# Kernel tuning notes

Hardware: AMD Instinct MI355X
Metric: run time of the kernel (lower is better)

## Reference

```python
import jax, jax.numpy as jnp
import numpy as np

N_NODES, N_EDGES, N_GRAPHS = 100000, 1600000, 1000
HID, GRP = 64, 10
LAMDA, EPS, T = 0.01, 1e-5, 2  # DiffGroupNorm lambda, BN eps, num_timesteps


def seg_softmax(logits, seg, num_segments):
    m = jax.ops.segment_max(logits, seg, num_segments=num_segments)
    e = jnp.exp(logits - m[seg])
    s = jax.ops.segment_sum(e, seg, num_segments=num_segments)
    return e / (s[seg] + 1e-16)


def gatv2(x_src, x_dst, src, dst, e_emb, Wl, bl, Wr, br, att, bias, n_dst):
    # GATv2Conv, heads=1, add_self_loops=False, negative_slope=0.01, aggr='add'
    xl = x_src @ Wl + bl                      # source transform (lin_l)
    xr = x_dst @ Wr + br                      # target transform (lin_r)
    m = xl[src] + xr[dst]                     # [E, C]
    if e_emb is not None:
        m = m + e_emb
    m = jnp.where(m > 0, m, 0.01 * m)         # leaky_relu(0.01)
    a = seg_softmax(m @ att, dst, n_dst)      # softmax over in-edges of each target
    out = jax.ops.segment_sum(xl[src] * a[:, None], dst, n_dst)
    return out + bias


def gru(xi, h, Wih, Whh, bih, bhh):
    gi = xi @ Wih.T + bih
    gh = h @ Whh.T + bhh
    ir, iz, inn = jnp.split(gi, 3, axis=-1)
    hr, hz, hn = jnp.split(gh, 3, axis=-1)
    r = jax.nn.sigmoid(ir + hr)
    z = jax.nn.sigmoid(iz + hz)
    n = jnp.tanh(inn + r * hn)
    return (1.0 - z) * n + z * h


def diff_group_norm(x, lin_W, lin_b, bn_w, bn_b):
    # PyG DiffGroupNorm (training-mode BatchNorm1d over groups*F)
    n, f = x.shape
    s = jax.nn.softmax(x @ lin_W + lin_b, axis=-1)            # [N, G]
    out = (s[:, :, None] * x[:, None, :]).reshape(n, GRP * f)  # [N, G*F]
    mean = out.mean(0)
    var = ((out - mean) ** 2).mean(0)
    out = (out - mean) / jnp.sqrt(var + EPS) * bn_w + bn_b
    out = out.reshape(n, GRP, f).sum(1)
    return x + LAMDA * out


def forward(x, edge_index, edge_attr, batch, pre_nW, pre_nb, pre_eW, pre_eb,
            g_Wl, g_Wl_b, g_Wr, g_Wr_b, g_We, g_att, g_bias,
            gru_Wih, gru_Whh, gru_bih, gru_bhh, gn_W, gn_b, bn_w, bn_b,
            ggat_Wl, ggat_Wl_b, ggat_Wr, ggat_Wr_b, ggat_att, ggat_bias,
            ggru_Wih, ggru_Whh, ggru_bih, ggru_bhh, ggn_W, ggn_b, gbn_w, gbn_b,
            post_W, post_b, out_W, out_b):
    src, dst = edge_index[0], edge_index[1]
    x = jax.nn.relu(x @ pre_nW + pre_nb)
    e = jax.nn.relu(edge_attr @ pre_eW + pre_eb)
    for l in range(g_Wl.shape[0]):            # layers_attention - 1 = 2 blocks
        e_emb = e @ g_We[l]                   # lin_edge (no bias)
        for _ in range(T):
            h = jax.nn.elu(gatv2(x, x, src, dst, e_emb, g_Wl[l], g_Wl_b[l],
                                 g_Wr[l], g_Wr_b[l], g_att[l], g_bias[l], N_NODES))
            x = jax.nn.relu(gru(h, x, gru_Wih[l], gru_Whh[l], gru_bih[l], gru_bhh[l]))
        x = diff_group_norm(x, gn_W[l], gn_b[l], bn_w[l], bn_b[l])
    # global readout: bipartite graph nodes -> graphs
    rsrc = jnp.arange(N_NODES)
    out = jax.nn.relu(jax.ops.segment_sum(x, batch, num_segments=N_GRAPHS))
    for _ in range(T):
        h = jax.nn.elu(gatv2(x, out, rsrc, batch, None, ggat_Wl, ggat_Wl_b,
                             ggat_Wr, ggat_Wr_b, ggat_att, ggat_bias, N_GRAPHS))
        out = jax.nn.relu(gru(h, out, ggru_Wih, ggru_Whh, ggru_bih, ggru_bhh))
    y = diff_group_norm(out, ggn_W, ggn_b, gbn_w, gbn_b)
    for l in range(post_W.shape[0]):
        y = jax.nn.relu(y @ post_W[l] + post_b[l])
    y = y @ out_W + out_b
    return y.reshape(-1)


def setup_inputs() -> dict:
    key = jax.random.key(0)
    ks = iter(jax.random.split(key, 64))
    Fin, Fe, H, L = 92, 50, HID, 2
    def nrm(shape, s=0.1):
        return jax.random.normal(next(ks), shape, jnp.float32) * s
    d = dict(
        x=jax.random.normal(next(ks), (N_NODES, Fin), jnp.float32),
        edge_index=jax.random.randint(next(ks), (2, N_EDGES), 0, N_NODES),
        edge_attr=jax.random.normal(next(ks), (N_EDGES, Fe), jnp.float32),
        batch=jnp.sort(jax.random.randint(next(ks), (N_NODES,), 0, N_GRAPHS)),
        pre_nW=nrm((Fin, H)), pre_nb=nrm((H,)),
        pre_eW=nrm((Fe, H)), pre_eb=nrm((H,)),
        g_Wl=nrm((L, H, H)), g_Wl_b=nrm((L, H)),
        g_Wr=nrm((L, H, H)), g_Wr_b=nrm((L, H)),
        g_We=nrm((L, H, H)), g_att=nrm((L, H)), g_bias=nrm((L, H)),
        gru_Wih=nrm((L, 3 * H, H)), gru_Whh=nrm((L, 3 * H, H)),
        gru_bih=nrm((L, 3 * H)), gru_bhh=nrm((L, 3 * H)),
        gn_W=nrm((L, H, GRP)), gn_b=nrm((L, GRP)),
        bn_w=jnp.ones((L, GRP * H), jnp.float32), bn_b=jnp.zeros((L, GRP * H), jnp.float32),
        ggat_Wl=nrm((H, H)), ggat_Wl_b=nrm((H,)),
        ggat_Wr=nrm((H, H)), ggat_Wr_b=nrm((H,)),
        ggat_att=nrm((H,)), ggat_bias=nrm((H,)),
        ggru_Wih=nrm((3 * H, H)), ggru_Whh=nrm((3 * H, H)),
        ggru_bih=nrm((3 * H,)), ggru_bhh=nrm((3 * H,)),
        ggn_W=nrm((H, GRP)), ggn_b=nrm((GRP,)),
        gbn_w=jnp.ones((GRP * H,), jnp.float32), gbn_b=jnp.zeros((GRP * H,), jnp.float32),
        post_W=nrm((2, H, H)), post_b=nrm((2, H)),
        out_W=nrm((H, 1)), out_b=nrm((1,)),
    )
    return d


def reference(x, edge_index, edge_attr, batch, pre_nW, pre_nb, pre_eW, pre_eb,
              g_Wl, g_Wl_b, g_Wr, g_Wr_b, g_We, g_att, g_bias,
              gru_Wih, gru_Whh, gru_bih, gru_bhh, gn_W, gn_b, bn_w, bn_b,
              ggat_Wl, ggat_Wl_b, ggat_Wr, ggat_Wr_b, ggat_att, ggat_bias,
              ggru_Wih, ggru_Whh, ggru_bih, ggru_bhh, ggn_W, ggn_b, gbn_w, gbn_b,
              post_W, post_b, out_W, out_b):
    return forward(x, edge_index, edge_attr, batch, pre_nW, pre_nb, pre_eW, pre_eb,
                   g_Wl, g_Wl_b, g_Wr, g_Wr_b, g_We, g_att, g_bias,
                   gru_Wih, gru_Whh, gru_bih, gru_bhh, gn_W, gn_b, bn_w, bn_b,
                   ggat_Wl, ggat_Wl_b, ggat_Wr, ggat_Wr_b, ggat_att, ggat_bias,
                   ggru_Wih, ggru_Whh, ggru_bih, ggru_bhh, ggn_W, ggn_b, gbn_w, gbn_b,
                   post_W, post_b, out_W, out_b)
```

## Files before the change

### kernel.cpp

```cpp
#include <hip/hip_runtime.h>
#include <hip/hip_bf16.h>

#define N_NODES 100000
#define N_EDGES 1600000
#define N_GRAPHS 1000
#define HID 64
#define GRP 10

typedef __attribute__((ext_vector_type(8))) short bf16x8;
typedef __attribute__((ext_vector_type(4))) float f32x4;

__device__ __forceinline__ float bf1(unsigned short u){ union{unsigned int x; float f;} v; v.x = ((unsigned int)u)<<16; return v.f; }
__device__ __forceinline__ float bf_lo(unsigned int u){ union{unsigned int x; float f;} v; v.x = u<<16; return v.f; }
__device__ __forceinline__ float bf_hi(unsigned int u){ union{unsigned int x; float f;} v; v.x = u & 0xFFFF0000u; return v.f; }
__device__ __forceinline__ unsigned short f2bf(float f){
  union{float f; unsigned int i;} v; v.f = f;
  unsigned int r = v.i + 0x7FFFu + ((v.i >> 16) & 1u);
  return (unsigned short)(r >> 16);
}
__device__ __forceinline__ float eluf(float v){ return v > 0.f ? v : expm1f(v); }
__device__ __forceinline__ float sigf(float v){ return 1.f/(1.f + expf(-v)); }

struct CvtEnt { const float* s; float* d; int rows; int cols; };
struct CvtArgs { CvtEnt e[16]; int cnt; };

__global__ __launch_bounds__(256) void k_convert(CvtArgs a){
  CvtEnt E = a.e[blockIdx.y];
  int n = E.rows * E.cols;
  for (int i = blockIdx.x*256 + threadIdx.x; i < n; i += gridDim.x*256){
    int r = i / E.cols, c = i % E.cols;
    E.d[(size_t)c*E.rows + r] = E.s[i];
  }
}

struct SpEnt { const float* s; unsigned short* dhi; unsigned short* dlo; int n; int k; int trans; };
struct SpArgs { SpEnt e[12]; int cnt; };

__global__ __launch_bounds__(256) void k_wsplit(SpArgs a){
  SpEnt E = a.e[blockIdx.y];
  int tot = E.n * E.k;
  for (int i = blockIdx.x*256 + threadIdx.x; i < tot; i += gridDim.x*256){
    int nr = i / E.k, kc = i - nr*E.k;
    float v = E.trans ? E.s[(size_t)kc*E.n + nr] : E.s[i];
    unsigned short hi = f2bf(v);
    unsigned short lo = f2bf(v - bf1(hi));
    E.dhi[i] = hi; E.dlo[i] = lo;
  }
}

__global__ __launch_bounds__(256) void k_wprep(const float* __restrict__ W1,
  const float* __restrict__ W2a, const float* __restrict__ W2b,
  unsigned short* __restrict__ W1Tb, unsigned short* __restrict__ W2Tba,
  unsigned short* __restrict__ W2Tbb)
{
  int i = blockIdx.x*256 + threadIdx.x;
  if (i >= 4096) return;
  int out = i & 63, k = i >> 6;
  int ks = k < 50 ? k : 0;
  unsigned short v1 = f2bf(W1[ks*64 + out]);
  if (k >= 50) v1 = 0;
  W1Tb [out*64 + k] = v1;
  W2Tba[out*64 + k] = f2bf(W2a[k*64 + out]);
  W2Tbb[out*64 + k] = f2bf(W2b[k*64 + out]);
}

__global__ __launch_bounds__(256) void k_hist(const int* __restrict__ dst, int* __restrict__ cnt){
  for (int e = blockIdx.x*256 + threadIdx.x; e < N_EDGES; e += gridDim.x*256)
    atomicAdd(cnt + dst[e], 1);
}

__global__ __launch_bounds__(256) void k_scan1(const int* __restrict__ cnt,
  int* __restrict__ excl, int* __restrict__ bsum, int N)
{
  __shared__ int sh[256];
  int t = threadIdx.x;
  int i = blockIdx.x*256 + t;
  int v = (i < N) ? cnt[i] : 0;
  sh[t] = v;
  __syncthreads();
  #pragma unroll
  for (int o=1;o<256;o<<=1){
    int x = (t>=o) ? sh[t-o] : 0;
    __syncthreads();
    sh[t] += x;
    __syncthreads();
  }
  if (i < N) excl[i] = sh[t] - v;
  if (t == 255) bsum[blockIdx.x] = sh[255];
}

__global__ __launch_bounds__(512) void k_scan2(const int* __restrict__ bsum,
  int* __restrict__ bo, int NB)
{
  __shared__ int sh[512];
  int t = threadIdx.x;
  int v = (t < NB) ? bsum[t] : 0;
  sh[t] = v;
  __syncthreads();
  #pragma unroll
  for (int o=1;o<512;o<<=1){
    int x = (t>=o) ? sh[t-o] : 0;
    __syncthreads();
    sh[t] += x;
    __syncthreads();
  }
  if (t < NB) bo[t] = sh[t] - v;
}

__global__ __launch_bounds__(256) void k_scan3(int* __restrict__ segoff,
  const int* __restrict__ bo, int* __restrict__ cursor, int N)
{
  int i = blockIdx.x*256 + threadIdx.x;
  if (i >= N) return;
  int v = segoff[i] + bo[i>>8];
  segoff[i] = v;
  cursor[i] = v;
  if (i == 0) segoff[N] = N_EDGES;
}

__global__ __launch_bounds__(256) void k_scatter(const int* __restrict__ src,
  const int* __restrict__ dst, int* __restrict__ cursor,
  int* __restrict__ srcp, int* __restrict__ perm)
{
  for (int e = blockIdx.x*256 + threadIdx.x; e < N_EDGES; e += gridDim.x*256){
    int d = dst[e];
    int pos = atomicAdd(cursor + d, 1);
    srcp[pos] = src[e];
    perm[pos] = e;
  }
}

__global__ __launch_bounds__(256) void k_goff(const int* __restrict__ batch, int* __restrict__ goff){
  for (int n = blockIdx.x*256 + threadIdx.x; n < N_NODES; n += gridDim.x*256){
    int b = batch[n];
    int prev = (n==0) ? -1 : batch[n-1];
    for (int g = prev+1; g <= b; g++) goff[g] = n;
    if (n == N_NODES-1){ for (int g=b+1; g<=N_GRAPHS; g++) goff[g] = N_NODES; }
  }
}

__global__ __launch_bounds__(256) void k_edge_emb(
  const float* __restrict__ EA, const int* __restrict__ perm,
  const unsigned short* __restrict__ W1Tb,
  const float* __restrict__ b1, const unsigned short* __restrict__ W2Tb,
  unsigned short* __restrict__ out, int nTiles)
{
  __shared__ float ea[64*50];
  __shared__ unsigned short hb[64*72];

  int tid = threadIdx.x;
  int lane = tid & 63;
  int wave = tid >> 6;
  int row16 = lane & 15;
  int kg = lane >> 4;

  bf16x8 w1[4][2], w2[4][2];
  #pragma unroll
  for (int n=0;n<4;n++){
    #pragma unroll
    for (int kk=0;kk<2;kk++){
      w1[n][kk] = *(const bf16x8*)(W1Tb + (n*16+row16)*64 + kk*32 + kg*8);
      w2[n][kk] = *(const bf16x8*)(W2Tb + (n*16+row16)*64 + kk*32 + kg*8);
    }
  }
  float bias[4];
  #pragma unroll
  for (int n=0;n<4;n++) bias[n] = b1[n*16+row16];

  int r = wave*16 + row16;
  float2 st[7];

  {
    long tile = blockIdx.x;
    if (tile < nTiles){
      #pragma unroll
      for (int k=0;k<7;k++){
        int j = tid + (k<<8);
        if (j < 1600){
          int row = j/25, c2 = j - row*25;
          int p = perm[tile*64 + row];
          st[k] = *(const float2*)(EA + (size_t)p*50 + (c2<<1));
        }
      }
    }
  }

  for (long t = blockIdx.x; t < nTiles; t += gridDim.x){
    #pragma unroll
    for (int k=0;k<7;k++){
      int j = tid + (k<<8);
      if (j < 1600){
        int row = j/25, c2 = j - row*25;
        *(float2*)(ea + row*50 + (c2<<1)) = st[k];
      }
    }
    __syncthreads();
    long tn = t + gridDim.x;
    if (tn < nTiles){
      #pragma unroll
      for (int k=0;k<7;k++){
        int j = tid + (k<<8);
        if (j < 1600){
          int row = j/25, c2 = j - row*25;
          int p = perm[tn*64 + row];
          st[k] = *(const float2*)(EA + (size_t)p*50 + (c2<<1));
        }
      }
    }

    bf16x8 a0, a1;
    {
      const float* p = ea + r*50;
      #pragma unroll
      for (int i=0;i<8;i++) ((short*)&a0)[i] = (short)f2bf(p[kg*8+i]);
      #pragma unroll
      for (int i=0;i<8;i++){
        int k = 32 + kg*8 + i;
        ((short*)&a1)[i] = (short)((k < 50) ? f2bf(p[k]) : (unsigned short)0);
      }
    }
    f32x4 c[4];
    #pragma unroll
    for (int n=0;n<4;n++){
      f32x4 acc = {0.f,0.f,0.f,0.f};
      acc = __builtin_amdgcn_mfma_f32_16x16x32_bf16(a0, w1[n][0], acc, 0,0,0);
      acc = __builtin_amdgcn_mfma_f32_16x16x32_bf16(a1, w1[n][1], acc, 0,0,0);
      c[n] = acc;
    }
    #pragma unroll
    for (int n=0;n<4;n++){
      #pragma unroll
      for (int q=0;q<4;q++){
        float v = fmaxf(c[n][q] + bias[n], 0.f);
        hb[(wave*16 + kg*4 + q)*72 + n*16 + row16] = f2bf(v);
      }
    }
    __syncthreads();

    bf16x8 ha = *(const bf16x8*)(hb + r*72 + kg*8);
    bf16x8 hc = *(const bf16x8*)(hb + r*72 + 32 + kg*8);
    f32x4 d[4];
    #pragma unroll
    for (int n=0;n<4;n++){
      f32x4 acc = {0.f,0.f,0.f,0.f};
      acc = __builtin_amdgcn_mfma_f32_16x16x32_bf16(ha, w2[n][0], acc, 0,0,0);
      acc = __builtin_amdgcn_mfma_f32_16x16x32_bf16(hc, w2[n][1], acc, 0,0,0);
      d[n] = acc;
    }
    __syncthreads();
    #pragma unroll
    for (int n=0;n<4;n++){
      #pragma unroll
      for (int q=0;q<4;q++)
        hb[(wave*16 + kg*4 + q)*72 + n*16 + row16] = f2bf(d[n][q]);
    }
    __syncthreads();

    {
      int rr = tid >> 2, q = tid & 3;
      const uint4* sp = (const uint4*)(hb + rr*72 + (q<<4));
      uint4 v0 = sp[0], v1 = sp[1];
      uint4* gp = (uint4*)(out + (t*64 + rr)*64 + (q<<4));
      gp[0] = v0; gp[1] = v1;
    }
  }
}

__device__ __forceinline__ void pack4(unsigned short* hi, unsigned short* lo, int ofs,
                                      float v0, float v1, float v2, float v3){
  unsigned short h0=f2bf(v0), h1=f2bf(v1), h2=f2bf(v2), h3=f2bf(v3);
  unsigned short l0=f2bf(v0-bf1(h0)), l1=f2bf(v1-bf1(h1)), l2=f2bf(v2-bf1(h2)), l3=f2bf(v3-bf1(h3));
  uint2 ph, pl;
  ph.x = ((unsigned int)h1<<16)|h0; ph.y = ((unsigned int)h3<<16)|h2;
  pl.x = ((unsigned int)l1<<16)|l0; pl.y = ((unsigned int)l3<<16)|l2;
  *(uint2*)(hi + ofs) = ph;
  *(uint2*)(lo + ofs) = pl;
}

template<int DUAL, int RELU>
__global__ __launch_bounds__(256) void k_lin_mfma(
  const float* __restrict__ X,
  const unsigned short* __restrict__ WAhi, const unsigned short* __restrict__ WAlo,
  const float* __restrict__ bA, float* __restrict__ outA,
  const unsigned short* __restrict__ WBhi, const unsigned short* __restrict__ WBlo,
  const float* __restrict__ bB, float* __restrict__ outB, int N)
{
  __shared__ unsigned short xh[64*72], xlo[64*72];
  int tid = threadIdx.x, lane = tid & 63, wave = tid >> 6;
  int col = lane & 15, kg = lane >> 4;
  long base = (long)blockIdx.x * 64;

  for (int idx = tid; idx < 1024; idx += 256){
    int r = idx >> 4, q = idx & 15;
    long row = base + r;
    float4 v = {0,0,0,0};
    if (row < N) v = ((const float4*)X)[row*16 + q];
    pack4(xh, xlo, r*72 + q*4, v.x, v.y, v.z, v.w);
  }
  __syncthreads();

  int r = wave*16 + col;
  bf16x8 ah[2], al[2];
  ah[0] = *(const bf16x8*)(xh  + r*72 + kg*8);
  ah[1] = *(const bf16x8*)(xh  + r*72 + 32 + kg*8);
  al[0] = *(const bf16x8*)(xlo + r*72 + kg*8);
  al[1] = *(const bf16x8*)(xlo + r*72 + 32 + kg*8);

  #pragma unroll
  for (int ct = 0; ct < 4; ct++){
    f32x4 aA = {0,0,0,0}, aB = {0,0,0,0};
    #pragma unroll
    for (int kk = 0; kk < 2; kk++){
      int wofs = (ct*16 + col)*64 + kk*32 + kg*8;
      bf16x8 bh = *(const bf16x8*)(WAhi + wofs);
      bf16x8 bl = *(const bf16x8*)(WAlo + wofs);
      aA = __builtin_amdgcn_mfma_f32_16x16x32_bf16(ah[kk], bh, aA, 0,0,0);
      aA = __builtin_amdgcn_mfma_f32_16x16x32_bf16(al[kk], bh, aA, 0,0,0);
      aA = __builtin_amdgcn_mfma_f32_16x16x32_bf16(ah[kk], bl, aA, 0,0,0);
      if (DUAL){
        bf16x8 ch = *(const bf16x8*)(WBhi + wofs);
        bf16x8 cl = *(const bf16x8*)(WBlo + wofs);
        aB = __builtin_amdgcn_mfma_f32_16x16x32_bf16(ah[kk], ch, aB, 0,0,0);
        aB = __builtin_amdgcn_mfma_f32_16x16x32_bf16(al[kk], ch, aB, 0,0,0);
        aB = __builtin_amdgcn_mfma_f32_16x16x32_bf16(ah[kk], cl, aB, 0,0,0);
      }
    }
    int c = ct*16 + col;
    float bAv = bA[c];
    float bBv = DUAL ? bB[c] : 0.f;
    #pragma unroll
    for (int reg = 0; reg < 4; reg++){
      long gr = base + wave*16 + kg*4 + reg;
      if (gr < N){
        float vA = aA[reg] + bAv;
        if (RELU) vA = fmaxf(vA, 0.f);
        outA[gr*64 + c] = vA;
        if (DUAL){
          float vB = aB[reg] + bBv;
          if (RELU) vB = fmaxf(vB, 0.f);
          outB[gr*64 + c] = vB;
        }
      }
    }
  }
}

__global__ __launch_bounds__(256) void k_gru_mfma(
  const float* __restrict__ agg, const float* __restrict__ gatb,
  float* __restrict__ x,
  const unsigned short* __restrict__ Wih_hi, const unsigned short* __restrict__ Wih_lo,
  const unsigned short* __restrict__ Whh_hi, const unsigned short* __restrict__ Whh_lo,
  const float* __restrict__ bih, const float* __restrict__ bhh, int N)
{
  __shared__ unsigned short hh_[64*72], hl_[64*72], xh_[64*72], xl_[64*72];
  int tid = threadIdx.x, lane = tid & 63, wave = tid >> 6;
  int col = lane & 15, kg = lane >> 4;
  long base = (long)blockIdx.x * 64;

  for (int idx = tid; idx < 1024; idx += 256){
    int r = idx >> 4, q = idx & 15;
    long row = base + r;
    float4 a = {0,0,0,0}, xx = {0,0,0,0};
    if (row < N){
      a  = ((const float4*)agg)[row*16 + q];
      xx = ((const float4*)x)[row*16 + q];
    }
    float h0 = eluf(a.x + gatb[q*4+0]);
    float h1 = eluf(a.y + gatb[q*4+1]);
    float h2 = eluf(a.z + gatb[q*4+2]);
    float h3 = eluf(a.w + gatb[q*4+3]);
    pack4(hh_, hl_, r*72 + q*4, h0, h1, h2, h3);
    pack4(xh_, xl_, r*72 + q*4, xx.x, xx.y, xx.z, xx.w);
  }
  __syncthreads();

  int r = wave*16 + col;
  bf16x8 hhi[2], hlo[2], xhi[2], xlo2[2];
  hhi[0] = *(const bf16x8*)(hh_ + r*72 + kg*8);
  hhi[1] = *(const bf16x8*)(hh_ + r*72 + 32 + kg*8);
  hlo[0] = *(const bf16x8*)(hl_ + r*72 + kg*8);
  hlo[1] = *(const bf16x8*)(hl_ + r*72 + 32 + kg*8);
  xhi[0] = *(const bf16x8*)(xh_ + r*72 + kg*8);
  xhi[1] = *(const bf16x8*)(xh_ + r*72 + 32 + kg*8);
  xlo2[0] = *(const bf16x8*)(xl_ + r*72 + kg*8);
  xlo2[1] = *(const bf16x8*)(xl_ + r*72 + 32 + kg*8);

  #pragma unroll
  for (int ct = 0; ct < 4; ct++){
    f32x4 ai[3], ah[3];
    #pragma unroll
    for (int g=0; g<3; g++){ ai[g] = (f32x4){0,0,0,0}; ah[g] = (f32x4){0,0,0,0}; }
    #pragma unroll
    for (int g = 0; g < 3; g++){
      int nt = g*4 + ct;
      #pragma unroll
      for (int kk = 0; kk < 2; kk++){
        int wofs = (nt*16 + col)*64 + kk*32 + kg*8;
        bf16x8 bh = *(const bf16x8*)(Wih_hi + wofs);
        bf16x8 bl = *(const bf16x8*)(Wih_lo + wofs);
        ai[g] = __builtin_amdgcn_mfma_f32_16x16x32_bf16(hhi[kk], bh, ai[g], 0,0,0);
        ai[g] = __builtin_amdgcn_mfma_f32_16x16x32_bf16(hlo[kk], bh, ai[g], 0,0,0);
        ai[g] = __builtin_amdgcn_mfma_f32_16x16x32_bf16(hhi[kk], bl, ai[g], 0,0,0);
        bf16x8 ch = *(const bf16x8*)(Whh_hi + wofs);
        bf16x8 cl = *(const bf16x8*)(Whh_lo + wofs);
        ah[g] = __builtin_amdgcn_mfma_f32_16x16x32_bf16(xhi[kk], ch, ah[g], 0,0,0);
        ah[g] = __builtin_amdgcn_mfma_f32_16x16x32_bf16(xlo2[kk], ch, ah[g], 0,0,0);
        ah[g] = __builtin_amdgcn_mfma_f32_16x16x32_bf16(xhi[kk], cl, ah[g], 0,0,0);
      }
    }
    int c = ct*16 + col;
    float bi0 = bih[c], bi1 = bih[64+c], bi2 = bih[128+c];
    float bh0 = bhh[c], bh1 = bhh[64+c], bh2 = bhh[128+c];
    #pragma unroll
    for (int reg = 0; reg < 4; reg++){
      int rr = wave*16 + kg*4 + reg;
      long gr = base + rr;
      float ir = ai[0][reg] + bi0, iz = ai[1][reg] + bi1, in2 = ai[2][reg] + bi2;
      float hr = ah[0][reg] + bh0, hz = ah[1][reg] + bh1, hn = ah[2][reg] + bh2;
      float xv = bf1(xh_[rr*72 + c]) + bf1(xl_[rr*72 + c]);
      float r_ = sigf(ir + hr);
      float z  = sigf(iz + hz);
      float nn = tanhf(in2 + r_*hn);
      float o = (1.f - z)*nn + z*xv;
      if (gr < N) x[gr*64 + c] = fmaxf(o, 0.f);
    }
  }
}

template<int K, int RELU, int INBF, int OUTBF, int HASB>
__global__ __launch_bounds__(256) void k_linear64(const void* Ap,
    const float* __restrict__ WT, const float* __restrict__ bias, void* Op, int N)
{
  int n = blockIdx.x*256 + threadIdx.x;
  if (n >= N) return;
  float a[K];
  if constexpr (INBF){
    const unsigned int* p = (const unsigned int*)((const unsigned short*)Ap + (size_t)n*K);
    #pragma unroll
    for (int i=0;i<K/2;i++){ unsigned int u=p[i]; a[2*i]=bf_lo(u); a[2*i+1]=bf_hi(u); }
  } else if constexpr (K % 4 == 0){
    const float4* p = (const float4*)((const float*)Ap + (size_t)n*K);
    #pragma unroll
    for (int i=0;i<K/4;i++){ float4 v=p[i]; a[4*i]=v.x; a[4*i+1]=v.y; a[4*i+2]=v.z; a[4*i+3]=v.w; }
  } else {
    const float2* p = (const float2*)((const float*)Ap + (size_t)n*K);
    #pragma unroll
    for (int i=0;i<K/2;i++){ float2 v=p[i]; a[2*i]=v.x; a[2*i+1]=v.y; }
  }
  for (int c=0;c<64;c+=4){
    float s0 = HASB ? bias[c+0] : 0.f;
    float s1 = HASB ? bias[c+1] : 0.f;
    float s2 = HASB ? bias[c+2] : 0.f;
    float s3 = HASB ? bias[c+3] : 0.f;
    const float* w = WT + (size_t)c*K;
    #pragma unroll
    for (int k=0;k<K;k++){
      float av = a[k];
      s0 = fmaf(av, w[k],     s0);
      s1 = fmaf(av, w[K+k],   s1);
      s2 = fmaf(av, w[2*K+k], s2);
      s3 = fmaf(av, w[3*K+k], s3);
    }
    if (RELU){ s0=fmaxf(s0,0.f); s1=fmaxf(s1,0.f); s2=fmaxf(s2,0.f); s3=fmaxf(s3,0.f); }
    if constexpr (OUTBF){
      uint2 uu;
      uu.x = ((unsigned int)f2bf(s1)<<16) | f2bf(s0);
      uu.y = ((unsigned int)f2bf(s3)<<16) | f2bf(s2);
      *(uint2*)((unsigned short*)Op + (size_t)n*64 + c) = uu;
    } else {
      float4 r; r.x=s0; r.y=s1; r.z=s2; r.w=s3;
      *(float4*)((float*)Op + (size_t)n*64 + c) = r;
    }
  }
}

template<int HASEMB, int IDSRC>
__global__ __launch_bounds__(256) void k_gat_fused(
  const int* __restrict__ srcp, const int* __restrict__ segoff,
  const float* __restrict__ xl, const float* __restrict__ xr,
  const unsigned short* __restrict__ emb, const float* __restrict__ att,
  float* __restrict__ agg, int nseg)
{
  int lane = threadIdx.x & 63;
  float av = att[lane];
  int wid = (blockIdx.x*256 + threadIdx.x) >> 6;
  int nw  = (gridDim.x*256) >> 6;
  for (int d = wid; d < nseg; d += nw){
    int e0 = segoff[d], e1 = segoff[d+1];
    float xrv = xr[(size_t)d*64 + lane];
    float m = -3.0e38f, s = 0.f, acc = 0.f;
    int e = e0;
    for (; e + 2 <= e1; e += 2){
      int sA = IDSRC ? e   : srcp[e];
      int sB = IDSRC ? e+1 : srcp[e+1];
      float xsA = xl[(size_t)sA*64 + lane];
      float xsB = xl[(size_t)sB*64 + lane];
      float vA = xsA + xrv, vB = xsB + xrv;
      if (HASEMB){
        vA += bf1(emb[(size_t)e*64 + lane]);
        vB += bf1(emb[(size_t)(e+1)*64 + lane]);
      }
      vA = vA > 0.f ? vA : 0.01f*vA;
      vB = vB > 0.f ? vB : 0.01f*vB;
      float pA = vA * av, pB = vB * av;
      #pragma unroll
      for (int o=32;o;o>>=1){ pA += __shfl_xor(pA, o, 64); pB += __shfl_xor(pB, o, 64); }
      float mn = fmaxf(m, fmaxf(pA, pB));
      float cm = expf(m - mn);
      float cA = expf(pA - mn);
      float cB = expf(pB - mn);
      s = fmaf(s, cm, cA + cB);
      acc = fmaf(acc, cm, fmaf(cA, xsA, cB*xsB));
      m = mn;
    }
    if (e < e1){
      int sN = IDSRC ? e : srcp[e];
      float xs = xl[(size_t)sN*64 + lane];
      float v = xs + xrv;
      if (HASEMB) v += bf1(emb[(size_t)e*64 + lane]);
      v = v > 0.f ? v : 0.01f*v;
      float p = v * av;
      #pragma unroll
      for (int o=32;o;o>>=1) p += __shfl_xor(p, o, 64);
      float mn = fmaxf(m, p);
      float cm = expf(m - mn);
      float cp = expf(p - mn);
      s   = fmaf(s, cm, cp);
      acc = fmaf(acc, cm, cp*xs);
      m = mn;
    }
    agg[(size_t)d*64 + lane] = acc / (s + 1e-16f);
  }
}

__global__ __launch_bounds__(256) void k_dgn_s(const float* __restrict__ x,
  const float* __restrict__ WT , const float* __restrict__ b,
  float* __restrict__ s, int N)
{
  int n = blockIdx.x*256 + threadIdx.x;
  if (n >= N) return;
  float a[64];
  const float4* p = (const float4*)(x + (size_t)n*64);
  #pragma unroll
  for (int i=0;i<16;i++){ float4 v=p[i]; a[4*i]=v.x; a[4*i+1]=v.y; a[4*i+2]=v.z; a[4*i+3]=v.w; }
  float lg[10];
  #pragma unroll
  for (int g=0; g<10; g++){
    float acc = b[g];
    const float* w = WT + (size_t)g*64;
    #pragma unroll
    for (int k=0;k<64;k++) acc = fmaf(a[k], w[k], acc);
    lg[g] = acc;
  }
  float m = lg[0];
  #pragma unroll
  for (int g=1;g<10;g++) m = fmaxf(m, lg[g]);
  float e[10], sum = 0.f;
  #pragma unroll
  for (int g=0;g<10;g++){ e[g] = expf(lg[g]-m); sum += e[g]; }
  float inv = 1.f/sum;
  #pragma unroll
  for (int g=0;g<10;g++) s[(size_t)n*10+g] = e[g]*inv;
}

__global__ __launch_bounds__(640) void k_dgn_stats(const float* __restrict__ s,
  const float* __restrict__ x, float* cs, float* cs2, int N)
{
  int g = threadIdx.x >> 6, f = threadIdx.x & 63;
  int per = (N + gridDim.x - 1) / gridDim.x;
  int n0 = blockIdx.x * per;
  int n1 = min(N, n0 + per);
  float a = 0.f, a2 = 0.f;
  for (int n = n0; n < n1; n++){
    float y = s[(size_t)n*10+g] * x[(size_t)n*64+f];
    a += y; a2 += y*y;
  }
  atomicAdd(&cs [g*64+f], a);
  atomicAdd(&cs2[g*64+f], a2);
}

__global__ void k_dgn_final(const float* cs, const float* cs2,
  const float* __restrict__ bw, const float* __restrict__ bb,
  float* scale, float* shiftsum, int N)
{
  __shared__ float sh[640];
  int i = threadIdx.x;
  float invN = 1.f / (float)N;
  float mean = cs[i]*invN;
  float var  = cs2[i]*invN - mean*mean;
  float sc = bw[i] / sqrtf(var + 1e-5f);
  scale[i] = sc;
  sh[i] = bb[i] - mean*sc;
  __syncthreads();
  if (i < 64){
    float t = 0.f;
    #pragma unroll
    for (int g=0;g<10;g++) t += sh[g*64+i];
    shiftsum[i] = t;
  }
}

__global__ __launch_bounds__(256) void k_dgn_apply(float* x,
  const float* __restrict__ s, const float* __restrict__ scale,
  const float* __restrict__ shiftsum, int N)
{
  int idx = blockIdx.x*256 + threadIdx.x;
  if (idx >= N*64) return;
  int n = idx >> 6, f = idx & 63;
  float ss = 0.f;
  #pragma unroll
  for (int g=0; g<10; g++) ss = fmaf(s[(size_t)n*10+g], scale[g*64+f], ss);
  float xvv = x[idx];
  x[idx] = xvv + 0.01f*(xvv*ss + shiftsum[f]);
}

__global__ __launch_bounds__(256) void k_gseg(const float* __restrict__ x,
  const int* __restrict__ goff, float* __restrict__ gout)
{
  int lane = threadIdx.x & 63;
  int wid = (blockIdx.x*256 + threadIdx.x) >> 6;
  int nw  = (gridDim.x*256) >> 6;
  for (int g = wid; g < N_GRAPHS; g += nw){
    int n0 = goff[g], n1 = goff[g+1];
    float acc = 0.f;
    for (int n = n0; n < n1; n++) acc += x[(size_t)n*64 + lane];
    gout[(size_t)g*64 + lane] = fmaxf(acc, 0.f);
  }
}

__global__ __launch_bounds__(256) void k_head(const float* __restrict__ y,
  const float* __restrict__ w, const float* __restrict__ b,
  float* __restrict__ out, int N)
{
  int n = blockIdx.x*256 + threadIdx.x;
  if (n >= N) return;
  float acc = b[0];
  const float4* p = (const float4*)(y + (size_t)n*64);
  #pragma unroll
  for (int i=0;i<16;i++){
    float4 v = p[i];
    acc = fmaf(v.x, w[4*i+0], acc);
    acc = fmaf(v.y, w[4*i+1], acc);
    acc = fmaf(v.z, w[4*i+2], acc);
    acc = fmaf(v.w, w[4*i+3], acc);
  }
  out[n] = acc;
}

extern "C" void kernel_launch(void* const* d_in, const int* in_sizes, int n_in,
                              void* d_out, int out_size, void* d_ws, size_t ws_size,
                              hipStream_t stream) {
  (void)in_sizes; (void)n_in; (void)out_size; (void)ws_size;

  char* base = (char*)d_ws; size_t off = 0;
  auto A = [&](size_t bytes)->void*{ void* p = base + off; off += (bytes + 255) & ~(size_t)255; return p; };
  unsigned short* e_emb = (unsigned short*)A((size_t)N_EDGES*64*2);
  float* xbuf   = (float*)A((size_t)N_NODES*64*4);
  float* xl     = (float*)A((size_t)N_NODES*64*4);
  float* xr     = (float*)A((size_t)N_NODES*64*4);
  float* agg    = (float*)A((size_t)N_NODES*64*4);
  int*   perm   = (int*)A((size_t)N_EDGES*4);
  int*   srcp   = (int*)A((size_t)N_EDGES*4);
  int*   segoff = (int*)A((size_t)(N_NODES+1)*4);
  int*   cursor = (int*)A((size_t)N_NODES*4);
  int*   bsum   = (int*)A(512*4);
  int*   bo     = (int*)A(512*4);
  int*   goff   = (int*)A((size_t)(N_GRAPHS+1)*4);
  float* sbuf   = (float*)A((size_t)N_NODES*10*4);
  float* gout   = (float*)A((size_t)N_GRAPHS*64*4);
  float* ybuf   = (float*)A((size_t)N_GRAPHS*64*4);
  float* ybuf2  = (float*)A((size_t)N_GRAPHS*64*4);
  float* colsum = (float*)A(2*640*4); float* colsumsq = colsum + 640;
  float* scale  = (float*)A((640+64)*4); float* shiftsum = scale + 640;
  unsigned short* W1Tb  = (unsigned short*)A(4096*2);
  unsigned short* W2Tb0 = (unsigned short*)A(4096*2);
  unsigned short* W2Tb1 = (unsigned short*)A(4096*2);
  unsigned short* LHI[5]; unsigned short* LLO[5];
  for (int i=0;i<5;i++){ LHI[i]=(unsigned short*)A(4096*2); LLO[i]=(unsigned short*)A(4096*2); }
  unsigned short* GHI[6]; unsigned short* GLO[6];
  for (int i=0;i<6;i++){ GHI[i]=(unsigned short*)A(12288*2); GLO[i]=(unsigned short*)A(12288*2); }
  float* wf     = (float*)A(60000*4);
  size_t wo = 0;
  auto W = [&](size_t n)->float*{ float* p = wf + wo; wo += n; return p; };

  float* pre_nWT = W(64*92);
  float* gnWT[2] = {W(640), W(640)};
  float* gWrT = W(4096);
  float* ggnWT = W(640);
  float* postWT[2] = {W(4096), W(4096)};

  const float* F[48];
  for (int i=0;i<41;i++) F[i] = (const float*)d_in[i];

  CvtArgs ca; ca.cnt = 0;
  auto addT = [&](const float* s, float* d, int r, int c){
    ca.e[ca.cnt].s=s; ca.e[ca.cnt].d=d; ca.e[ca.cnt].rows=r; ca.e[ca.cnt].cols=c; ca.cnt++; };

  addT(F[4],  pre_nWT, 92, 64);
  for (int l=0;l<2;l++) addT(F[19] + l*640,  gnWT[l], 64, 10);
  addT(F[25], gWrT, 64, 64);
  addT(F[33], ggnWT, 64, 10);
  for (int l=0;l<2;l++) addT(F[37] + l*4096, postWT[l], 64, 64);

  SpArgs sa; sa.cnt = 0;
  auto addS = [&](const float* s, unsigned short* dhi, unsigned short* dlo, int n, int k, int tr){
    sa.e[sa.cnt].s=s; sa.e[sa.cnt].dhi=dhi; sa.e[sa.cnt].dlo=dlo;
    sa.e[sa.cnt].n=n; sa.e[sa.cnt].k=k; sa.e[sa.cnt].trans=tr; sa.cnt++; };
  for (int l=0;l<2;l++) addS(F[8]  + l*4096, LHI[l],   LLO[l],   64, 64, 1);
  for (int l=0;l<2;l++) addS(F[10] + l*4096, LHI[2+l], LLO[2+l], 64, 64, 1);
  addS(F[23], LHI[4], LLO[4], 64, 64, 1);
  for (int l=0;l<2;l++) addS(F[15] + l*12288, GHI[l],   GLO[l],   192, 64, 0);
  for (int l=0;l<2;l++) addS(F[16] + l*12288, GHI[2+l], GLO[2+l], 192, 64, 0);
  addS(F[29], GHI[4], GLO[4], 192, 64, 0);
  addS(F[30], GHI[5], GLO[5], 192, 64, 0);

  const int* src   = (const int*)d_in[1];
  const int* dst   = src + N_EDGES;
  const int* batch = (const int*)d_in[3];

  const int NBn = (N_NODES + 255)/256;
  const int NBg = (N_GRAPHS + 255)/256;
  const int NBa = (N_NODES*64)/256;
  const int NTIL = N_EDGES/64;
  const int NBt = (N_NODES + 63)/64;
  const int NBtg = (N_GRAPHS + 63)/64;

  k_convert<<<dim3(24, ca.cnt), 256, 0, stream>>>(ca);
  k_wsplit<<<dim3(8, sa.cnt), 256, 0, stream>>>(sa);
  k_wprep<<<16,256,0,stream>>>(F[6], F[12], F[12]+4096, W1Tb, W2Tb0, W2Tb1);

  hipMemsetAsync(cursor, 0, (size_t)N_NODES*4, stream);
  k_hist<<<2048,256,0,stream>>>(dst, cursor);
  k_scan1<<<NBn,256,0,stream>>>(cursor, segoff, bsum, N_NODES);
  k_scan2<<<1,512,0,stream>>>(bsum, bo, NBn);
  k_scan3<<<NBn,256,0,stream>>>(segoff, bo, cursor, N_NODES);
  k_scatter<<<2048,256,0,stream>>>(src, dst, cursor, srcp, perm);
  k_goff<<<NBn,256,0,stream>>>(batch, goff);

  k_linear64<92,1,0,0,1><<<NBn,256,0,stream>>>(F[0], pre_nWT, F[5], xbuf, N_NODES);

  for (int l=0; l<2; l++){
    k_edge_emb<<<4096,256,0,stream>>>(F[2], perm, W1Tb, F[7], (l==0)?W2Tb0:W2Tb1, e_emb, NTIL);

    for (int t=0; t<2; t++){
      k_lin_mfma<1,0><<<NBt,256,0,stream>>>(xbuf,
          LHI[l], LLO[l], F[9] + l*64, xl,
          LHI[2+l], LLO[2+l], F[11] + l*64, xr, N_NODES);
      k_gat_fused<1,0><<<4096,256,0,stream>>>(srcp, segoff, xl, xr, e_emb,
                                              F[13] + l*64, agg, N_NODES);
      k_gru_mfma<<<NBt,256,0,stream>>>(agg, F[14] + l*64, xbuf,
          GHI[l], GLO[l], GHI[2+l], GLO[2+l],
          F[17] + l*192, F[18] + l*192, N_NODES);
    }
    hipMemsetAsync(colsum, 0, 2*640*4, stream);
    k_dgn_s<<<NBn,256,0,stream>>>(xbuf, gnWT[l], F[20] + l*10, sbuf, N_NODES);
    k_dgn_stats<<<512,640,0,stream>>>(sbuf, xbuf, colsum, colsumsq, N_NODES);
    k_dgn_final<<<1,640,0,stream>>>(colsum, colsumsq, F[21] + l*640, F[22] + l*640, scale, shiftsum, N_NODES);
    k_dgn_apply<<<NBa,256,0,stream>>>(xbuf, sbuf, scale, shiftsum, N_NODES);
  }

  k_gseg<<<250,256,0,stream>>>(xbuf, goff, gout);

  k_lin_mfma<0,0><<<NBt,256,0,stream>>>(xbuf, LHI[4], LLO[4], F[24], xl,
                                        nullptr, nullptr, nullptr, nullptr, N_NODES);
  for (int t=0; t<2; t++){
    k_linear64<64,0,0,0,1><<<NBg,256,0,stream>>>(gout, gWrT, F[26], xr, N_GRAPHS);
    k_gat_fused<0,1><<<256,256,0,stream>>>(nullptr, goff, xl, xr, nullptr,
                                           F[27], agg, N_GRAPHS);
    k_gru_mfma<<<NBtg,256,0,stream>>>(agg, F[28], gout,
        GHI[4], GLO[4], GHI[5], GLO[5], F[31], F[32], N_GRAPHS);
  }

  hipMemsetAsync(colsum, 0, 2*640*4, stream);
  k_dgn_s<<<NBg,256,0,stream>>>(gout, ggnWT, F[34], sbuf, N_GRAPHS);
  k_dgn_stats<<<8,640,0,stream>>>(sbuf, gout, colsum, colsumsq, N_GRAPHS);
  k_dgn_final<<<1,640,0,stream>>>(colsum, colsumsq, F[35], F[36], scale, shiftsum, N_GRAPHS);
  k_dgn_apply<<<(N_GRAPHS*64+255)/256,256,0,stream>>>(gout, sbuf, scale, shiftsum, N_GRAPHS);

  k_linear64<64,1,0,0,1><<<NBg,256,0,stream>>>(gout, postWT[0], F[38],      ybuf,  N_GRAPHS);
  k_linear64<64,1,0,0,1><<<NBg,256,0,stream>>>(ybuf, postWT[1], F[38] + 64, ybuf2, N_GRAPHS);
  k_head<<<NBg,256,0,stream>>>(ybuf2, F[39], F[40], (float*)d_out, N_GRAPHS);
}
```

Measured before the change: 2.930 ms.

## Read edge attrs contiguously with scattered emb writes; split GAT lanes across four edges

```diff
diff --git a/kernel.cpp b/kernel.cpp
--- a/kernel.cpp
+++ b/kernel.cpp
@@ -120,13 +120,13 @@
 
 __global__ __launch_bounds__(256) void k_scatter(const int* __restrict__ src,
   const int* __restrict__ dst, int* __restrict__ cursor,
-  int* __restrict__ srcp, int* __restrict__ perm)
+  int* __restrict__ srcp, int* __restrict__ ipos)
 {
   for (int e = blockIdx.x*256 + threadIdx.x; e < N_EDGES; e += gridDim.x*256){
     int d = dst[e];
     int pos = atomicAdd(cursor + d, 1);
     srcp[pos] = src[e];
-    perm[pos] = e;
+    ipos[e] = pos;
   }
 }
 
@@ -140,7 +140,7 @@
 }
 
 __global__ __launch_bounds__(256) void k_edge_emb(
-  const float* __restrict__ EA, const int* __restrict__ perm,
+  const float* __restrict__ EA, const int* __restrict__ ipos,
   const unsigned short* __restrict__ W1Tb,
   const float* __restrict__ b1, const unsigned short* __restrict__ W2Tb,
   unsigned short* __restrict__ out, int nTiles)
@@ -168,43 +168,34 @@
   for (int n=0;n<4;n++) bias[n] = b1[n*16+row16];
 
   int r = wave*16 + row16;
-  float2 st[7];
+  float4 st[4];
 
   {
-    long tile = blockIdx.x;
-    if (tile < nTiles){
+    long t0 = blockIdx.x;
+    if (t0 < nTiles){
+      const float4* gp = (const float4*)(EA + t0*3200);
       #pragma unroll
-      for (int k=0;k<7;k++){
+      for (int k=0;k<4;k++){
         int j = tid + (k<<8);
-        if (j < 1600){
-          int row = j/25, c2 = j - row*25;
-          int p = perm[tile*64 + row];
-          st[k] = *(const float2*)(EA + (size_t)p*50 + (c2<<1));
-        }
+        if (j < 800) st[k] = gp[j];
       }
     }
   }
 
   for (long t = blockIdx.x; t < nTiles; t += gridDim.x){
     #pragma unroll
-    for (int k=0;k<7;k++){
+    for (int k=0;k<4;k++){
       int j = tid + (k<<8);
-      if (j < 1600){
-        int row = j/25, c2 = j - row*25;
-        *(float2*)(ea + row*50 + (c2<<1)) = st[k];
-      }
+      if (j < 800) ((float4*)ea)[j] = st[k];
     }
     __syncthreads();
     long tn = t + gridDim.x;
     if (tn < nTiles){
+      const float4* gp = (const float4*)(EA + tn*3200);
       #pragma unroll
-      for (int k=0;k<7;k++){
+      for (int k=0;k<4;k++){
         int j = tid + (k<<8);
-        if (j < 1600){
-          int row = j/25, c2 = j - row*25;
-          int p = perm[tn*64 + row];
-          st[k] = *(const float2*)(EA + (size_t)p*50 + (c2<<1));
-        }
+        if (j < 800) st[k] = gp[j];
       }
     }
 
@@ -258,10 +249,11 @@
 
     {
       int rr = tid >> 2, q = tid & 3;
+      int ip = ipos[t*64 + rr];
       const uint4* sp = (const uint4*)(hb + rr*72 + (q<<4));
       uint4 v0 = sp[0], v1 = sp[1];
-      uint4* gp = (uint4*)(out + (t*64 + rr)*64 + (q<<4));
-      gp[0] = v0; gp[1] = v1;
+      uint4* gq = (uint4*)(out + (size_t)ip*64 + (q<<4));
+      gq[0] = v0; gq[1] = v1;
     }
   }
 }
@@ -482,54 +474,68 @@
   float* __restrict__ agg, int nseg)
 {
   int lane = threadIdx.x & 63;
-  float av = att[lane];
+  int grp = lane >> 4;
+  int sq  = lane & 15;
+  float4 av = ((const float4*)att)[sq];
   int wid = (blockIdx.x*256 + threadIdx.x) >> 6;
   int nw  = (gridDim.x*256) >> 6;
   for (int d = wid; d < nseg; d += nw){
     int e0 = segoff[d], e1 = segoff[d+1];
-    float xrv = xr[(size_t)d*64 + lane];
-    float m = -3.0e38f, s = 0.f, acc = 0.f;
-    int e = e0;
-    for (; e + 2 <= e1; e += 2){
-      int sA = IDSRC ? e   : srcp[e];
-      int sB = IDSRC ? e+1 : srcp[e+1];
-      float xsA = xl[(size_t)sA*64 + lane];
-      float xsB = xl[(size_t)sB*64 + lane];
-      float vA = xsA + xrv, vB = xsB + xrv;
+    float4 xrv = ((const float4*)(xr + (size_t)d*64))[sq];
+    float m = -3.0e38f, s = 0.f;
+    float4 acc = {0.f,0.f,0.f,0.f};
+    for (int eb = e0; eb < e1; eb += 4){
+      int e = eb + grp;
+      bool act = e < e1;
+      int ee = act ? e : e0;
+      int sN = IDSRC ? ee : srcp[ee];
+      float4 xs = ((const float4*)(xl + (size_t)sN*64))[sq];
+      float4 v;
+      v.x = xs.x + xrv.x; v.y = xs.y + xrv.y;
+      v.z = xs.z + xrv.z; v.w = xs.w + xrv.w;
       if (HASEMB){
-        vA += bf1(emb[(size_t)e*64 + lane]);
-        vB += bf1(emb[(size_t)(e+1)*64 + lane]);
+        uint2 u = *(const uint2*)(emb + (size_t)ee*64 + (sq<<2));
+        v.x += bf_lo(u.x); v.y += bf_hi(u.x);
+        v.z += bf_lo(u.y); v.w += bf_hi(u.y);
       }
-      vA = vA > 0.f ? vA : 0.01f*vA;
-      vB = vB > 0.f ? vB : 0.01f*vB;
-      float pA = vA * av, pB = vB * av;
-      #pragma unroll
-      for (int o=32;o;o>>=1){ pA += __shfl_xor(pA, o, 64); pB += __shfl_xor(pB, o, 64); }
-      float mn = fmaxf(m, fmaxf(pA, pB));
-      float cm = expf(m - mn);
-      float cA = expf(pA - mn);
-      float cB = expf(pB - mn);
-      s = fmaf(s, cm, cA + cB);
-      acc = fmaf(acc, cm, fmaf(cA, xsA, cB*xsB));
-      m = mn;
-    }
-    if (e < e1){
-      int sN = IDSRC ? e : srcp[e];
-      float xs = xl[(size_t)sN*64 + lane];
-      float v = xs + xrv;
-      if (HASEMB) v += bf1(emb[(size_t)e*64 + lane]);
-      v = v > 0.f ? v : 0.01f*v;
-      float p = v * av;
-      #pragma unroll
-      for (int o=32;o;o>>=1) p += __shfl_xor(p, o, 64);
+      v.x = v.x > 0.f ? v.x : 0.01f*v.x;
+      v.y = v.y > 0.f ? v.y : 0.01f*v.y;
+      v.z = v.z > 0.f ? v.z : 0.01f*v.z;
+      v.w = v.w > 0.f ? v.w : 0.01f*v.w;
+      float p = v.x*av.x;
+      p = fmaf(v.y, av.y, p);
+      p = fmaf(v.z, av.z, p);
+      p = fmaf(v.w, av.w, p);
+      p += __shfl_xor(p, 1, 64);
+      p += __shfl_xor(p, 2, 64);
+      p += __shfl_xor(p, 4, 64);
+      p += __shfl_xor(p, 8, 64);
+      if (!act) p = -3.0e38f;
       float mn = fmaxf(m, p);
       float cm = expf(m - mn);
-      float cp = expf(p - mn);
-      s   = fmaf(s, cm, cp);
-      acc = fmaf(acc, cm, cp*xs);
+      float cp = act ? expf(p - mn) : 0.f;
+      s = fmaf(s, cm, cp);
+      acc.x = fmaf(acc.x, cm, cp*xs.x);
+      acc.y = fmaf(acc.y, cm, cp*xs.y);
+      acc.z = fmaf(acc.z, cm, cp*xs.z);
+      acc.w = fmaf(acc.w, cm, cp*xs.w);
       m = mn;
     }
-    agg[(size_t)d*64 + lane] = acc / (s + 1e-16f);
+    float mo = fmaxf(m, __shfl_xor(m, 16, 64));
+    float M  = fmaxf(mo, __shfl_xor(mo, 32, 64));
+    float w  = expf(m - M);
+    s *= w; acc.x *= w; acc.y *= w; acc.z *= w; acc.w *= w;
+    s += __shfl_xor(s, 16, 64);  s += __shfl_xor(s, 32, 64);
+    acc.x += __shfl_xor(acc.x, 16, 64); acc.x += __shfl_xor(acc.x, 32, 64);
+    acc.y += __shfl_xor(acc.y, 16, 64); acc.y += __shfl_xor(acc.y, 32, 64);
+    acc.z += __shfl_xor(acc.z, 16, 64); acc.z += __shfl_xor(acc.z, 32, 64);
+    acc.w += __shfl_xor(acc.w, 16, 64); acc.w += __shfl_xor(acc.w, 32, 64);
+    if (grp == 0){
+      float inv = 1.f/(s + 1e-16f);
+      float4 o;
+      o.x = acc.x*inv; o.y = acc.y*inv; o.z = acc.z*inv; o.w = acc.w*inv;
+      ((float4*)(agg + (size_t)d*64))[sq] = o;
+    }
   }
 }
 
@@ -659,7 +665,7 @@
   float* xl     = (float*)A((size_t)N_NODES*64*4);
   float* xr     = (float*)A((size_t)N_NODES*64*4);
   float* agg    = (float*)A((size_t)N_NODES*64*4);
-  int*   perm   = (int*)A((size_t)N_EDGES*4);
+  int*   ipos   = (int*)A((size_t)N_EDGES*4);
   int*   srcp   = (int*)A((size_t)N_EDGES*4);
   int*   segoff = (int*)A((size_t)(N_NODES+1)*4);
   int*   cursor = (int*)A((size_t)N_NODES*4);
@@ -734,13 +740,13 @@
   k_scan1<<<NBn,256,0,stream>>>(cursor, segoff, bsum, N_NODES);
   k_scan2<<<1,512,0,stream>>>(bsum, bo, NBn);
   k_scan3<<<NBn,256,0,stream>>>(segoff, bo, cursor, N_NODES);
-  k_scatter<<<2048,256,0,stream>>>(src, dst, cursor, srcp, perm);
+  k_scatter<<<2048,256,0,stream>>>(src, dst, cursor, srcp, ipos);
   k_goff<<<NBn,256,0,stream>>>(batch, goff);
 
   k_linear64<92,1,0,0,1><<<NBn,256,0,stream>>>(F[0], pre_nWT, F[5], xbuf, N_NODES);
 
   for (int l=0; l<2; l++){
-    k_edge_emb<<<4096,256,0,stream>>>(F[2], perm, W1Tb, F[7], (l==0)?W2Tb0:W2Tb1, e_emb, NTIL);
+    k_edge_emb<<<4096,256,0,stream>>>(F[2], ipos, W1Tb, F[7], (l==0)?W2Tb0:W2Tb1, e_emb, NTIL);
 
     for (int t=0; t<2; t++){
       k_lin_mfma<1,0><<<NBt,256,0,stream>>>(xbuf,
```

Result: faster. 2.667 ms (-9.0%).
